# Kernel optimization log

Hardware: AMD Instinct MI355X
Metric: run time of the kernel (lower is better)

Reference implementation:

```python
import jax, jax.numpy as jnp
import numpy as np

B, T, E, H = 4, 1024, 1024, 16
D = E // H  # head_size = 64
EPS = 1e-5


def layernorm(x, g, b):
    mu = jnp.mean(x, axis=-1, keepdims=True)
    var = jnp.mean(jnp.square(x - mu), axis=-1, keepdims=True)
    return (x - mu) * jax.lax.rsqrt(var + EPS) * g + b


def setup_inputs() -> dict:
    key = jax.random.key(0)
    ks = jax.random.split(key, 12)
    s = 0.02
    return {
        "x": jax.random.normal(ks[0], (B, T, E), dtype=jnp.float32),
        "ln1_g": jnp.ones((E,), jnp.float32),
        "ln1_b": jnp.zeros((E,), jnp.float32),
        "Wq": jax.random.normal(ks[1], (H, E, D), dtype=jnp.float32) * s,
        "Wk": jax.random.normal(ks[2], (H, E, D), dtype=jnp.float32) * s,
        "Wv": jax.random.normal(ks[3], (H, E, D), dtype=jnp.float32) * s,
        "Wp": jax.random.normal(ks[4], (E, E), dtype=jnp.float32) * s,
        "bp": jnp.zeros((E,), jnp.float32),
        "ln2_g": jnp.ones((E,), jnp.float32),
        "ln2_b": jnp.zeros((E,), jnp.float32),
        "W1": jax.random.normal(ks[5], (E, 4 * E), dtype=jnp.float32) * s,
        "b1": jnp.zeros((4 * E,), jnp.float32),
        "W2": jax.random.normal(ks[6], (4 * E, E), dtype=jnp.float32) * s,
        "b2": jnp.zeros((E,), jnp.float32),
    }


def reference(x, ln1_g, ln1_b, Wq, Wk, Wv, Wp, bp, ln2_g, ln2_b, W1, b1, W2, b2):
    # --- attention sub-block (pre-LN) ---
    h = layernorm(x, ln1_g, ln1_b)               # [B,T,E]
    q = jnp.einsum('bte,hed->bhtd', h, Wq)       # [B,H,T,D]
    k = jnp.einsum('bte,hed->bhtd', h, Wk)
    v = jnp.einsum('bte,hed->bhtd', h, Wv)
    # NOTE: original module has NO 1/sqrt(D) scaling and its 'tril' buffer is
    # all-ones, so masked_fill is a no-op -> full (non-causal) softmax.
    scores = jnp.einsum('bhtd,bhsd->bhts', q, k)  # [B,H,T,T]
    attn = jax.nn.softmax(scores, axis=-1)
    o = jnp.einsum('bhts,bhsd->bhtd', attn, v)    # [B,H,T,D]
    o = o.transpose(0, 2, 1, 3).reshape(x.shape[0], x.shape[1], -1)  # [B,T,E]
    x = x + o @ Wp + bp
    # --- feedforward sub-block (dropout is identity at eval) ---
    h2 = layernorm(x, ln2_g, ln2_b)
    x = x + jax.nn.relu(h2 @ W1 + b1) @ W2 + b2
    return x
```

## Files before the change

kernel.cpp:

```cpp
#include <hip/hip_runtime.h>
#include <hip/hip_bf16.h>

#define BB 4
#define TT 1024
#define EE 1024
#define HH 16
#define DD 64
#define MM 4096
#define NQKV 3072
#define E4 4096

using short8  = __attribute__((ext_vector_type(8))) short;
using short4v = __attribute__((ext_vector_type(4))) short;
using f32x4   = __attribute__((ext_vector_type(4))) float;

__device__ __forceinline__ short f2bf(float f) {
    __hip_bfloat16 h = __float2bfloat16(f);
    return *reinterpret_cast<short*>(&h);
}

__device__ __forceinline__ float bf2f(short s) {
    unsigned int u = ((unsigned int)(unsigned short)s) << 16;
    return __uint_as_float(u);
}

__device__ __forceinline__ unsigned int cvtpk_bf16(float a, float b) {
    unsigned int w;
    asm("v_cvt_pk_bf16_f32 %0, %1, %2" : "=v"(w) : "v"(a), "v"(b));
    return w;
}

__device__ __forceinline__ void gld16(const void* g, void* l) {
    __builtin_amdgcn_global_load_lds((__attribute__((address_space(1))) void*)g,
                                     (__attribute__((address_space(3))) void*)l,
                                     16, 0, 0);
}

__device__ __forceinline__ void tcvt_tile(const float* __restrict__ in,
                                          short* __restrict__ out,
                                          int R, int C, int r0, int c0) {
    __shared__ short tile[64][65];
    const int tr = threadIdx.x >> 6;
    const int tc = threadIdx.x & 63;
#pragma unroll
    for (int i = 0; i < 16; ++i) {
        int r = i * 4 + tr;
        tile[tc][r] = f2bf(in[(size_t)(r0 + r) * C + c0 + tc]);
    }
    __syncthreads();
#pragma unroll
    for (int i = 0; i < 16; ++i) {
        int c = i * 4 + tr;
        out[(size_t)(c0 + c) * R + r0 + tc] = tile[c][tc];
    }
}

__global__ __launch_bounds__(256) void packs_kernel(const float* __restrict__ Wq,
                                                    const float* __restrict__ Wk,
                                                    const float* __restrict__ Wv,
                                                    const float* __restrict__ Wp,
                                                    const float* __restrict__ W1,
                                                    const float* __restrict__ W2,
                                                    short* __restrict__ wqkv,
                                                    short* __restrict__ wp_bf,
                                                    short* __restrict__ w1_bf,
                                                    short* __restrict__ w2_bf) {
    const int blk = blockIdx.x;
    if (blk < 768) {
        __shared__ short tile[64][65];
        const int m = blk >> 4;
        const int which = m >> 4, head = m & 15;
        const float* src = ((which == 0) ? Wq : (which == 1) ? Wk : Wv) +
                           (size_t)head * EE * DD;
        const float scale = (which == 1) ? 1.44269504f : 1.0f;
        const int e0 = (blk & 15) * 64;
        const int tr = threadIdx.x >> 6, tc = threadIdx.x & 63;
#pragma unroll
        for (int i = 0; i < 16; ++i) {
            int e = i * 4 + tr;
            tile[tc][e] = f2bf(src[(size_t)(e0 + e) * DD + tc] * scale);
        }
        __syncthreads();
#pragma unroll
        for (int i = 0; i < 16; ++i) {
            int d = i * 4 + tr;
            wqkv[(size_t)(which * 1024 + head * 64 + d) * EE + e0 + tc] = tile[d][tc];
        }
    } else if (blk < 1024) {
        const int idx = blk - 768;
        tcvt_tile(Wp, wp_bf, EE, EE, (idx >> 4) * 64, (idx & 15) * 64);
    } else if (blk < 2048) {
        const int idx = blk - 1024;
        tcvt_tile(W1, w1_bf, EE, E4, (idx >> 6) * 64, (idx & 63) * 64);
    } else {
        const int idx = blk - 2048;
        tcvt_tile(W2, w2_bf, E4, EE, (idx >> 4) * 64, (idx & 15) * 64);
    }
}

__global__ __launch_bounds__(256) void vtr_kernel(const short* __restrict__ qkv,
                                                  short* __restrict__ vT) {
    __shared__ short tile[64][68];
    const int b = blockIdx.z;
    const int t0 = blockIdx.x * 64, c0 = blockIdx.y * 64;
    const int tr = threadIdx.x >> 4;
    const int q4 = (threadIdx.x & 15) * 4;
#pragma unroll
    for (int i = 0; i < 4; ++i) {
        int t = i * 16 + tr;
        short4v v = *(const short4v*)&qkv[((size_t)b * TT + t0 + t) * NQKV + 2048 + c0 + q4];
        *(short4v*)&tile[t][q4] = v;
    }
    __syncthreads();
#pragma unroll
    for (int i = 0; i < 4; ++i) {
        int c = i * 16 + tr;
        short4v v;
        v[0] = tile[q4 + 0][c];
        v[1] = tile[q4 + 1][c];
        v[2] = tile[q4 + 2][c];
        v[3] = tile[q4 + 3][c];
        *(short4v*)&vT[((size_t)b * 1024 + c0 + c) * TT + t0 + q4] = v;
    }
}

__global__ __launch_bounds__(256) void ln_kernel(const float* __restrict__ x,
                                                 const float* __restrict__ g,
                                                 const float* __restrict__ b,
                                                 short* __restrict__ out) {
    __shared__ float red[4];
    const int row = blockIdx.x;
    const int tid = threadIdx.x;
    float4 v = *(const float4*)&x[(size_t)row * EE + tid * 4];
    float s = v.x + v.y + v.z + v.w;
#pragma unroll
    for (int off = 32; off >= 1; off >>= 1) s += __shfl_xor(s, off, 64);
    if ((tid & 63) == 0) red[tid >> 6] = s;
    __syncthreads();
    float mean = (red[0] + red[1] + red[2] + red[3]) * (1.0f / EE);
    __syncthreads();
    float d0 = v.x - mean, d1 = v.y - mean, d2 = v.z - mean, d3 = v.w - mean;
    s = d0 * d0 + d1 * d1 + d2 * d2 + d3 * d3;
#pragma unroll
    for (int off = 32; off >= 1; off >>= 1) s += __shfl_xor(s, off, 64);
    if ((tid & 63) == 0) red[tid >> 6] = s;
    __syncthreads();
    float var = (red[0] + red[1] + red[2] + red[3]) * (1.0f / EE);
    float rstd = rsqrtf(var + 1e-5f);
    int c = tid * 4;
    short4v o;
    o[0] = f2bf(d0 * rstd * g[c + 0] + b[c + 0]);
    o[1] = f2bf(d1 * rstd * g[c + 1] + b[c + 1]);
    o[2] = f2bf(d2 * rstd * g[c + 2] + b[c + 2]);
    o[3] = f2bf(d3 * rstd * g[c + 3] + b[c + 3]);
    *(short4v*)&out[(size_t)row * EE + c] = o;
}

__global__ __launch_bounds__(256) void redk4_kernel(const short* __restrict__ parts,
                                                    const float* __restrict__ bias,
                                                    const float* __restrict__ resid,
                                                    float* __restrict__ out) {
    const size_t i = ((size_t)blockIdx.x * 256 + threadIdx.x) * 4;
    float4 r = *(const float4*)&resid[i];
    float4 bb = *(const float4*)&bias[i & 1023];
    float acc0 = r.x + bb.x, acc1 = r.y + bb.y, acc2 = r.z + bb.z, acc3 = r.w + bb.w;
#pragma unroll
    for (int z = 0; z < 4; ++z) {
        short4v p = *(const short4v*)&parts[(size_t)z * MM * EE + i];
        acc0 += bf2f(p[0]);
        acc1 += bf2f(p[1]);
        acc2 += bf2f(p[2]);
        acc3 += bf2f(p[3]);
    }
    float4 o;
    o.x = acc0; o.y = acc1; o.z = acc2; o.w = acc3;
    *(float4*)&out[i] = o;
}

template <bool HAS_BIAS, bool RELU, bool SPLIT>
__global__ __launch_bounds__(512, 2) void gemm256(const short* __restrict__ A,
                                                  const short* __restrict__ Bt,
                                                  const float* __restrict__ bias,
                                                  void* __restrict__ outp,
                                                  int M, int N, int K, int lda) {
    __shared__ __align__(16) short Ab[2][2][8192];
    __shared__ __align__(16) short Bb[2][2][8192];

    const int tid = threadIdx.x;
    const int lane = tid & 63;
    const int wid = tid >> 6;
    const int wr = wid >> 2;
    const int wc = wid & 3;
    const int l15 = lane & 15, lhi = lane >> 4;
    const int rsw = l15 & 7;

    int wg = blockIdx.y * gridDim.x + blockIdx.x;
    const int chunk = (gridDim.x * gridDim.y) >> 3;
    wg = (wg & 7) * chunk + (wg >> 3);
    const int bx = wg % gridDim.x, by = wg / gridDim.x;
    const int row0 = by * 256, col0 = bx * 256;

    const int kb = SPLIT ? blockIdx.z * K : 0;

    const int srow = tid >> 3;
    const int scol = (((tid & 7) ^ (srow & 7)) << 3);

    const int NT = K >> 6;

    f32x4 acc[8][4] = {};

    auto stageA = [&](int b, int h, int k0) {
#pragma unroll
        for (int j = 0; j < 2; ++j)
            gld16(&A[(size_t)(row0 + h * 128 + j * 64 + srow) * lda + kb + k0 + scol],
                  &Ab[b][h][j * 4096 + wid * 512]);
    };
    auto stageB = [&](int b, int h, int k0) {
#pragma unroll
        for (int j = 0; j < 2; ++j)
            gld16(&Bt[(size_t)(col0 + h * 128 + j * 64 + srow) * lda + kb + k0 + scol],
                  &Bb[b][h][j * 4096 + wid * 512]);
    };

    stageA(0, 0, 0); stageA(0, 1, 0);
    stageB(0, 0, 0); stageB(0, 1, 0);
    if (NT > 1) {
        stageB(1, 0, 64); stageB(1, 1, 64);
        asm volatile("s_waitcnt vmcnt(4)" ::: "memory");
    } else {
        asm volatile("s_waitcnt vmcnt(0)" ::: "memory");
    }
    __builtin_amdgcn_s_barrier();

    for (int u = 0; u < NT; ++u) {
        const int buf = u & 1;
        short8 bfr[4][2];
#pragma unroll
        for (int p = 0; p < 4; ++p) {
            if (p == 0) {
#pragma unroll
                for (int n = 0; n < 4; ++n)
#pragma unroll
                    for (int ks = 0; ks < 2; ++ks)
                        bfr[n][ks] = *(const short8*)&Bb[buf][wc >> 1]
                            [((wc & 1) * 64 + n * 16 + l15) * 64 +
                             (((ks << 2) + lhi) ^ rsw) * 8];
            }
            short8 af[2][2];
#pragma unroll
            for (int mi = 0; mi < 2; ++mi)
#pragma unroll
                for (int ks = 0; ks < 2; ++ks)
                    af[mi][ks] = *(const short8*)&Ab[buf][wr]
                        [((p * 2 + mi) * 16 + l15) * 64 +
                         (((ks << 2) + lhi) ^ rsw) * 8];
            if (p == 0 && u + 1 < NT) stageA(buf ^ 1, 0, (u + 1) << 6);
            if (p == 1 && u + 1 < NT) stageA(buf ^ 1, 1, (u + 1) << 6);
            if (p == 2 && u + 2 < NT) stageB(buf, 0, (u + 2) << 6);
            if (p == 3 && u + 2 < NT) stageB(buf, 1, (u + 2) << 6);
            __builtin_amdgcn_s_barrier();
            __builtin_amdgcn_s_setprio(1);
#pragma unroll
            for (int mi = 0; mi < 2; ++mi)
#pragma unroll
                for (int n = 0; n < 4; ++n)
#pragma unroll
                    for (int ks = 0; ks < 2; ++ks)
                        acc[p * 2 + mi][n] = __builtin_amdgcn_mfma_f32_16x16x32_bf16(
                            af[mi][ks], bfr[n][ks], acc[p * 2 + mi][n], 0, 0, 0);
            __builtin_amdgcn_s_setprio(0);
            if (p == 3 && u + 1 < NT) {
                if (u + 2 < NT) asm volatile("s_waitcnt vmcnt(4)" ::: "memory");
                else            asm volatile("s_waitcnt vmcnt(0)" ::: "memory");
            }
            __builtin_amdgcn_s_barrier();
        }
    }

    short* outb = (short*)outp;
    if (SPLIT) outb += (size_t)blockIdx.z * M * N;
#pragma unroll
    for (int m = 0; m < 8; ++m)
#pragma unroll
        for (int n = 0; n < 4; ++n)
#pragma unroll
            for (int r = 0; r < 4; ++r) {
                int row = row0 + wr * 128 + m * 16 + lhi * 4 + r;
                int col = col0 + wc * 64 + n * 16 + l15;
                float v = acc[m][n][r];
                if (!SPLIT) {
                    if (HAS_BIAS) v += bias[col];
                    if (RELU) v = fmaxf(v, 0.f);
                }
                outb[(size_t)row * N + col] = f2bf(v);
            }
}

template <int BN, int PIPE, bool HAS_BIAS, bool RELU, bool RESID, bool OUT_BF16>
__global__ __launch_bounds__(256) void gemm_bt(const short* __restrict__ A,
                                               const short* __restrict__ Bt,
                                               const float* __restrict__ bias,
                                               const float* __restrict__ resid,
                                               void* __restrict__ outp,
                                               int M, int N, int K) {
    constexpr int WRC = (BN == 128) ? 2 : 4;
    constexpr int WCC = (BN == 128) ? 2 : 1;
    constexpr int MI = 8 / WRC;
    constexpr int NI = BN / (16 * WCC);
    constexpr int BCH = BN / 32;
    constexpr int ASZ = 128 * 64, BSZ = BN * 64;

    __shared__ __align__(16) short As[(PIPE ? 2 : 1) * ASZ];
    __shared__ __align__(16) short Bs[(PIPE ? 2 : 1) * BSZ];

    const int tid = threadIdx.x;
    const int lane = tid & 63;
    const int wid = tid >> 6;
    const int wr = (WRC == 2) ? (wid >> 1) : wid;
    const int wc = (WCC == 2) ? (wid & 1) : 0;
    const int l15 = lane & 15, lhi = lane >> 4;

    int wg = blockIdx.y * gridDim.x + blockIdx.x;
    const int chunk = (gridDim.x * gridDim.y) >> 3;
    wg = (wg & 7) * chunk + (wg >> 3);
    const int bx = wg % gridDim.x;
    const int by = wg / gridDim.x;
    const int row0 = by * 128, col0 = bx * BN;

    const int srow = tid >> 3;
    const int scol = (((tid & 7) ^ (srow & 7)) << 3);
    const int rsw = l15 & 7;

    const int wrow0 = wr * (16 * MI);
    const int wcol0 = wc * (16 * NI);

    f32x4 acc[MI][NI] = {};

    auto stage = [&](int k0, int bs) {
#pragma unroll
        for (int ch = 0; ch < 4; ++ch)
            gld16(&A[(size_t)(row0 + ch * 32 + srow) * K + k0 + scol],
                  &As[bs * ASZ + ch * 2048 + wid * 512]);
#pragma unroll
        for (int ch = 0; ch < BCH; ++ch)
            gld16(&Bt[(size_t)(col0 + ch * 32 + srow) * K + k0 + scol],
                  &Bs[bs * BSZ + ch * 2048 + wid * 512]);
    };
    auto compute = [&](int bs) {
#pragma unroll
        for (int ks = 0; ks < 2; ++ks) {
            short8 af[MI], bf[NI];
#pragma unroll
            for (int mi = 0; mi < MI; ++mi)
                af[mi] = *(const short8*)&As[bs * ASZ + (wrow0 + mi * 16 + l15) * 64 +
                                             (((ks << 2) + lhi) ^ rsw) * 8];
#pragma unroll
            for (int ni = 0; ni < NI; ++ni)
                bf[ni] = *(const short8*)&Bs[bs * BSZ + (wcol0 + ni * 16 + l15) * 64 +
                                             (((ks << 2) + lhi) ^ rsw) * 8];
#pragma unroll
            for (int mi = 0; mi < MI; ++mi)
#pragma unroll
                for (int ni = 0; ni < NI; ++ni)
                    acc[mi][ni] = __builtin_amdgcn_mfma_f32_16x16x32_bf16(
                        af[mi], bf[ni], acc[mi][ni], 0, 0, 0);
        }
    };

    if (PIPE == 1) {
        const int nt = K >> 6;
        stage(0, 0);
        stage(64, 1);
        int cur = 0;
        for (int t = 0; t < nt; ++t) {
            if (t + 1 < nt) asm volatile("s_waitcnt vmcnt(6)" ::: "memory");
            else            asm volatile("s_waitcnt vmcnt(0)" ::: "memory");
            __builtin_amdgcn_s_barrier();
            __builtin_amdgcn_sched_barrier(0);
            compute(cur);
            __builtin_amdgcn_sched_barrier(0);
            __builtin_amdgcn_s_barrier();
            if (t + 2 < nt) stage((t + 2) << 6, cur);
            cur ^= 1;
        }
    } else {
        for (int k0 = 0; k0 < K; k0 += 64) {
            __syncthreads();
            stage(k0, 0);
            __syncthreads();
            compute(0);
        }
    }

    float* outf = (float*)outp;
    short* outb = (short*)outp;
#pragma unroll
    for (int mi = 0; mi < MI; ++mi)
#pragma unroll
        for (int ni = 0; ni < NI; ++ni)
#pragma unroll
            for (int r = 0; r < 4; ++r) {
                int row = row0 + wrow0 + mi * 16 + lhi * 4 + r;
                int col = col0 + wcol0 + ni * 16 + l15;
                float v = acc[mi][ni][r];
                if (HAS_BIAS) v += bias[col];
                if (RELU) v = fmaxf(v, 0.f);
                if (RESID) v += resid[(size_t)row * N + col];
                if (OUT_BF16) outb[(size_t)row * N + col] = f2bf(v);
                else outf[(size_t)row * N + col] = v;
            }
}

__global__ __launch_bounds__(512) void attn_kernel(const short* __restrict__ qkv,
                                                   const short* __restrict__ vT,
                                                   short* __restrict__ obuf) {
    __shared__ __align__(16) short Ks[2][128 * 64];
    __shared__ __align__(16) short Vs[2][64 * 128];
    __shared__ __align__(16) unsigned int Pl[8][16][44];
    const int tid = threadIdx.x;
    const int lane = tid & 63;
    const int wid = tid >> 6;
    const int l15 = lane & 15, lhi = lane >> 4;
    const int lhi4 = lhi * 4;

    const int nb = ((blockIdx.x & 7) << 5) + (blockIdx.x >> 3);
    const int b = nb >> 6;
    const int h = (nb >> 2) & 15;
    const int q0 = (nb & 3) << 8;
    const size_t rbase = (size_t)b * TT;
    const int hq = h * 64;
    const short* vg = vT + ((size_t)b * 1024 + hq) * TT;

    const int srow = tid >> 3;
    const int scol = (((tid & 7) ^ (srow & 7)) << 3);
    const int vrow = tid >> 4;
    const int vscol = ((tid & 15) ^ (vrow & 7)) << 3;
    const int rsw = l15 & 7;

    short8 aq[2][2];
#pragma unroll
    for (int g = 0; g < 2; ++g)
#pragma unroll
        for (int ks = 0; ks < 2; ++ks)
            aq[g][ks] = *(const short8*)&qkv[(rbase + q0 + wid * 32 + g * 16 + l15) * NQKV +
                                             hq + ks * 32 + lhi * 8];

    f32x4 psum[2] = {};
    f32x4 o[2][4] = {};

    auto stage = [&](int buf, int st) {
#pragma unroll
        for (int ch = 0; ch < 2; ++ch)
            gld16(&qkv[(rbase + st + ch * 64 + srow) * NQKV + 1024 + hq + scol],
                  &Ks[buf][ch * 4096 + wid * 512]);
#pragma unroll
        for (int ch = 0; ch < 2; ++ch)
            gld16(&vg[(size_t)(ch * 32 + vrow) * TT + st + vscol],
                  &Vs[buf][ch * 4096 + wid * 512]);
    };

    stage(0, 0);
    __syncthreads();

    int cur = 0;
    for (int st = 0; st < TT; st += 128) {
        if (st + 128 < TT) stage(cur ^ 1, st + 128);
        const short* K = &Ks[cur][0];
        const short* V = &Vs[cur][0];

#pragma unroll
        for (int h2 = 0; h2 < 2; ++h2) {
            short8 kf[4][2];
#pragma unroll
            for (int nt = 0; nt < 4; ++nt)
#pragma unroll
                for (int ks = 0; ks < 2; ++ks)
                    kf[nt][ks] = *(const short8*)&K[(h2 * 64 + nt * 16 + l15) * 64 +
                                                   (((ks << 2) + lhi) ^ rsw) * 8];

            short8 pa[2][2];
#pragma unroll
            for (int g = 0; g < 2; ++g) {
                f32x4 stv[4] = {};
                __builtin_amdgcn_s_setprio(1);
#pragma unroll
                for (int nt = 0; nt < 4; ++nt)
#pragma unroll
                    for (int ks = 0; ks < 2; ++ks)
                        stv[nt] = __builtin_amdgcn_mfma_f32_16x16x32_bf16(
                            kf[nt][ks], aq[g][ks], stv[nt], 0, 0, 0);
                __builtin_amdgcn_s_setprio(0);
#pragma unroll
                for (int nt = 0; nt < 4; ++nt) {
                    f32x4 pv;
#pragma unroll
                    for (int r = 0; r < 4; ++r) pv[r] = exp2f(stv[nt][r]);
                    psum[g] += pv;
                    uint2 ww;
                    ww.x = cvtpk_bf16(pv[0], pv[1]);
                    ww.y = cvtpk_bf16(pv[2], pv[3]);
                    *(uint2*)&Pl[wid][l15][nt * 8 + lhi * 2] = ww;
                }
                pa[g][0] = *(const short8*)&Pl[wid][l15][lhi4];
                pa[g][1] = *(const short8*)&Pl[wid][l15][16 + lhi4];
            }

            short8 vf[4][2];
#pragma unroll
            for (int dt = 0; dt < 4; ++dt)
#pragma unroll
                for (int k2 = 0; k2 < 2; ++k2)
                    vf[dt][k2] = *(const short8*)&V[(dt * 16 + l15) * 128 +
                                                   ((h2 << 3) + (((k2 << 2) + lhi) ^ rsw)) * 8];
            __builtin_amdgcn_s_setprio(1);
#pragma unroll
            for (int g = 0; g < 2; ++g)
#pragma unroll
                for (int dt = 0; dt < 4; ++dt)
#pragma unroll
                    for (int k2 = 0; k2 < 2; ++k2)
                        o[g][dt] = __builtin_amdgcn_mfma_f32_16x16x32_bf16(
                            pa[g][k2], vf[dt][k2], o[g][dt], 0, 0, 0);
            __builtin_amdgcn_s_setprio(0);
        }

        __syncthreads();
        cur ^= 1;
    }
#pragma unroll
    for (int g = 0; g < 2; ++g) {
        float ls = (psum[g][0] + psum[g][1]) + (psum[g][2] + psum[g][3]);
        ls += __shfl_xor(ls, 16, 64);
        ls += __shfl_xor(ls, 32, 64);
        float inv = 1.0f / ls;
        float i0 = __shfl(inv, lhi4 + 0, 64);
        float i1 = __shfl(inv, lhi4 + 1, 64);
        float i2 = __shfl(inv, lhi4 + 2, 64);
        float i3 = __shfl(inv, lhi4 + 3, 64);
#pragma unroll
        for (int dt = 0; dt < 4; ++dt) {
            int col = hq + dt * 16 + l15;
            size_t rw = rbase + q0 + wid * 32 + g * 16 + lhi4;
            obuf[(rw + 0) * EE + col] = f2bf(o[g][dt][0] * i0);
            obuf[(rw + 1) * EE + col] = f2bf(o[g][dt][1] * i1);
            obuf[(rw + 2) * EE + col] = f2bf(o[g][dt][2] * i2);
            obuf[(rw + 3) * EE + col] = f2bf(o[g][dt][3] * i3);
        }
    }
}

extern "C" void kernel_launch(void* const* d_in, const int* in_sizes, int n_in,
                              void* d_out, int out_size, void* d_ws, size_t ws_size,
                              hipStream_t stream) {
    const float* x   = (const float*)d_in[0];
    const float* g1  = (const float*)d_in[1];
    const float* be1 = (const float*)d_in[2];
    const float* Wq  = (const float*)d_in[3];
    const float* Wk  = (const float*)d_in[4];
    const float* Wv  = (const float*)d_in[5];
    const float* Wp  = (const float*)d_in[6];
    const float* bp  = (const float*)d_in[7];
    const float* g2  = (const float*)d_in[8];
    const float* be2 = (const float*)d_in[9];
    const float* W1  = (const float*)d_in[10];
    const float* b1f = (const float*)d_in[11];
    const float* W2  = (const float*)d_in[12];
    const float* b2f = (const float*)d_in[13];

    char* p = (char*)d_ws;
    short* h_bf   = (short*)p; p += (size_t)MM * EE * 2;
    short* wqkv   = (short*)p; p += (size_t)EE * NQKV * 2;
    short* qkv    = (short*)p; p += (size_t)MM * NQKV * 2;
    short* o_bf   = (short*)p; p += (size_t)MM * EE * 2;
    short* wp_bf  = (short*)p; p += (size_t)EE * EE * 2;
    float* x1     = (float*)p; p += (size_t)MM * EE * 4;
    short* h2_bf  = (short*)p; p += (size_t)MM * EE * 2;
    short* w1_bf  = (short*)p; p += (size_t)EE * E4 * 2;
    short* mid_bf = (short*)p; p += (size_t)MM * E4 * 2;
    short* w2_bf  = (short*)p; p += (size_t)E4 * EE * 2;
    short* vTb    = (short*)p; p += (size_t)BB * 1024 * TT * 2;

    short* parts = (short*)d_ws;

    packs_kernel<<<3072, 256, 0, stream>>>(Wq, Wk, Wv, Wp, W1, W2,
                                           wqkv, wp_bf, w1_bf, w2_bf);

    ln_kernel<<<MM, 256, 0, stream>>>(x, g1, be1, h_bf);

    gemm256<false, false, false>
        <<<dim3(NQKV / 256, MM / 256), 512, 0, stream>>>(h_bf, wqkv, nullptr,
                                                         qkv, MM, NQKV, EE, EE);

    vtr_kernel<<<dim3(16, 16, BB), 256, 0, stream>>>(qkv, vTb);

    attn_kernel<<<BB * HH * (TT / 256), 512, 0, stream>>>(qkv, vTb, o_bf);

    gemm_bt<64, 1, true, false, true, false>
        <<<dim3(EE / 64, MM / 128), 256, 0, stream>>>(o_bf, wp_bf, bp, x, x1, MM, EE, EE);

    ln_kernel<<<MM, 256, 0, stream>>>(x1, g2, be2, h2_bf);

    gemm256<true, true, false>
        <<<dim3(E4 / 256, MM / 256), 512, 0, stream>>>(h2_bf, w1_bf, b1f,
                                                       mid_bf, MM, E4, EE, EE);

    gemm256<false, false, true>
        <<<dim3(EE / 256, MM / 256, 4), 512, 0, stream>>>(mid_bf, w2_bf, nullptr,
                                                          parts, MM, EE, 1024, E4);
    redk4_kernel<<<(MM * EE / 4) / 256, 256, 0, stream>>>(parts, b2f, x1,
                                                          (float*)d_out);
}
```

Measured before the change: 199.7 us.

## Double-buffer A fragments in registers to overlap LDS reads with MFMA

Restructures the GEMM inner K-loop so the next A fragment is read from LDS into a second register set while MFMAs run on the current one. The number of barriers per K-tile drops from eight to four. This aims to hide LDS read latency behind matrix-core work. It raises register pressure and changes the barrier and staging order, which could reduce occupancy or create hazards between the LDS buffers being staged and those being read.

```diff
diff --git a/kernel.cpp b/kernel.cpp
--- a/kernel.cpp
+++ b/kernel.cpp
@@ -232,49 +232,60 @@
     }
     __builtin_amdgcn_s_barrier();
 
+    short8 bfr[4][2], afA[2][2], afB[2][2];
+
+    auto ldbfr = [&](int buf) {
+#pragma unroll
+        for (int n = 0; n < 4; ++n)
+#pragma unroll
+            for (int ks = 0; ks < 2; ++ks)
+                bfr[n][ks] = *(const short8*)&Bb[buf][wc >> 1]
+                    [((wc & 1) * 64 + n * 16 + l15) * 64 +
+                     (((ks << 2) + lhi) ^ rsw) * 8];
+    };
+    auto ldaf = [&](short8 dst[2][2], int buf, int p) {
+#pragma unroll
+        for (int mi = 0; mi < 2; ++mi)
+#pragma unroll
+            for (int ks = 0; ks < 2; ++ks)
+                dst[mi][ks] = *(const short8*)&Ab[buf][wr]
+                    [((p * 2 + mi) * 16 + l15) * 64 +
+                     (((ks << 2) + lhi) ^ rsw) * 8];
+    };
+    auto domfma = [&](short8 src[2][2], int p) {
+        __builtin_amdgcn_s_setprio(1);
+#pragma unroll
+        for (int mi = 0; mi < 2; ++mi)
+#pragma unroll
+            for (int n = 0; n < 4; ++n)
+#pragma unroll
+                for (int ks = 0; ks < 2; ++ks)
+                    acc[p * 2 + mi][n] = __builtin_amdgcn_mfma_f32_16x16x32_bf16(
+                        src[mi][ks], bfr[n][ks], acc[p * 2 + mi][n], 0, 0, 0);
+        __builtin_amdgcn_s_setprio(0);
+    };
+
     for (int u = 0; u < NT; ++u) {
         const int buf = u & 1;
-        short8 bfr[4][2];
-#pragma unroll
-        for (int p = 0; p < 4; ++p) {
-            if (p == 0) {
-#pragma unroll
-                for (int n = 0; n < 4; ++n)
-#pragma unroll
-                    for (int ks = 0; ks < 2; ++ks)
-                        bfr[n][ks] = *(const short8*)&Bb[buf][wc >> 1]
-                            [((wc & 1) * 64 + n * 16 + l15) * 64 +
-                             (((ks << 2) + lhi) ^ rsw) * 8];
-            }
-            short8 af[2][2];
-#pragma unroll
-            for (int mi = 0; mi < 2; ++mi)
-#pragma unroll
-                for (int ks = 0; ks < 2; ++ks)
-                    af[mi][ks] = *(const short8*)&Ab[buf][wr]
-                        [((p * 2 + mi) * 16 + l15) * 64 +
-                         (((ks << 2) + lhi) ^ rsw) * 8];
-            if (p == 0 && u + 1 < NT) stageA(buf ^ 1, 0, (u + 1) << 6);
-            if (p == 1 && u + 1 < NT) stageA(buf ^ 1, 1, (u + 1) << 6);
-            if (p == 2 && u + 2 < NT) stageB(buf, 0, (u + 2) << 6);
-            if (p == 3 && u + 2 < NT) stageB(buf, 1, (u + 2) << 6);
-            __builtin_amdgcn_s_barrier();
-            __builtin_amdgcn_s_setprio(1);
-#pragma unroll
-            for (int mi = 0; mi < 2; ++mi)
-#pragma unroll
-                for (int n = 0; n < 4; ++n)
-#pragma unroll
-                    for (int ks = 0; ks < 2; ++ks)
-                        acc[p * 2 + mi][n] = __builtin_amdgcn_mfma_f32_16x16x32_bf16(
-                            af[mi][ks], bfr[n][ks], acc[p * 2 + mi][n], 0, 0, 0);
-            __builtin_amdgcn_s_setprio(0);
-            if (p == 3 && u + 1 < NT) {
-                if (u + 2 < NT) asm volatile("s_waitcnt vmcnt(4)" ::: "memory");
-                else            asm volatile("s_waitcnt vmcnt(0)" ::: "memory");
-            }
-            __builtin_amdgcn_s_barrier();
-        }
+        ldbfr(buf);
+        ldaf(afA, buf, 0);
+        if (u + 1 < NT) stageA(buf ^ 1, 0, (u + 1) << 6);
+        ldaf(afB, buf, 1);
+        domfma(afA, 0);
+        __builtin_amdgcn_s_barrier();
+        if (u + 1 < NT) stageA(buf ^ 1, 1, (u + 1) << 6);
+        ldaf(afA, buf, 2);
+        domfma(afB, 1);
+        __builtin_amdgcn_s_barrier();
+        if (u + 2 < NT) stageB(buf, 0, (u + 2) << 6);
+        ldaf(afB, buf, 3);
+        domfma(afA, 2);
+        __builtin_amdgcn_s_barrier();
+        if (u + 2 < NT) stageB(buf, 1, (u + 2) << 6);
+        domfma(afB, 3);
+        if (u + 2 < NT)      asm volatile("s_waitcnt vmcnt(4)" ::: "memory");
+        else if (u + 1 < NT) asm volatile("s_waitcnt vmcnt(0)" ::: "memory");
+        __builtin_amdgcn_s_barrier();
     }
 
     short* outb = (short*)outp;
```

Measured after the change: 219.0 us. +9.7%, slower.
